# Kernel optimization log

Measured on AMD Instinct MI355X. Metric: run time of the kernel, lower is better.

Reference implementation:

```python
import jax, jax.numpy as jnp
import numpy as np

BIG = 1000000.0


def setup_inputs() -> dict:
    key = jax.random.key(0)
    k1, k2 = jax.random.split(key)
    embeddings = jax.random.normal(k1, (8192, 128), dtype=jnp.float32)
    labels = jax.random.randint(k2, (8192,), 0, 512, dtype=jnp.int64)
    return {"embeddings": embeddings, "labels": labels, "margin": jnp.float32(0.5)}


def _pairwise_euclidean(x):
    # [N, N] Euclidean distance matrix, numerically safe sqrt (zero diag)
    sq = jnp.sum(x * x, axis=1)
    d2 = sq[:, None] + sq[None, :] - 2.0 * (x @ x.T)
    d2 = jnp.maximum(d2, 0.0)
    nz = d2 > 0.0
    return jnp.where(nz, jnp.sqrt(jnp.where(nz, d2, 1.0)), 0.0)


def reference(embeddings, labels, margin):
    n = embeddings.shape[0]
    dist = _pairwise_euclidean(embeddings)                      # [N, N]
    same = (labels[:, None] == labels[None, :]).astype(dist.dtype)
    mask_pos = same - jnp.eye(n, dtype=dist.dtype)              # positives, excl. self
    mask_neg = 1.0 - same                                       # different label
    pos_dist = jnp.max(dist * mask_pos, axis=1)                 # hardest positive
    neg_dist = jnp.min(dist + (1.0 - mask_neg) * BIG, axis=1)   # hardest negative
    loss = jax.nn.relu(pos_dist - neg_dist + margin)
    return jnp.mean(loss)
```

## Files before the change

kernel.cpp:

```cpp
#include <hip/hip_runtime.h>

#define NROW 8192
#define DIM  128
#define NSEG 16
#define NBLK (64 * NSEG)
#define BIGF 1e30f

typedef __attribute__((ext_vector_type(8))) short bf16x8;
typedef __attribute__((ext_vector_type(4))) float f32x4;


__device__ __forceinline__ unsigned short f2bf(float f) {
    unsigned u = __float_as_uint(f);
    unsigned r = (u + 0x7fffu + ((u >> 16) & 1u)) >> 16;
    return (unsigned short)r;
}

__device__ __forceinline__ void gload_lds16(const void* g, void* l) {
    __builtin_amdgcn_global_load_lds(
        (const __attribute__((address_space(1))) void*)g,
        (__attribute__((address_space(3))) void*)l, 16, 0, 0);
}

__global__ __launch_bounds__(256) void prep_kernel(const float* __restrict__ x,
                                                   unsigned short* __restrict__ xb2,
                                                   float* __restrict__ sq,
                                                   float* __restrict__ out) {
    const int t   = threadIdx.x;
    const int row = blockIdx.x * 16 + (t >> 4);
    const int c   = t & 15;
    if (blockIdx.x == 0 && t == 0) out[0] = 0.0f;
    const float* xr = x + (size_t)row * DIM + c * 8;
    float4 f0 = *(const float4*)xr;
    float4 f1 = *(const float4*)(xr + 4);
    float s = f0.x*f0.x + f0.y*f0.y + f0.z*f0.z + f0.w*f0.w
            + f1.x*f1.x + f1.y*f1.y + f1.z*f1.z + f1.w*f1.w;
    #pragma unroll
    for (int m = 1; m <= 8; m <<= 1) s += __shfl_xor(s, m);
    unsigned w0 = (unsigned)f2bf(f0.x) | ((unsigned)f2bf(f0.y) << 16);
    unsigned w1 = (unsigned)f2bf(f0.z) | ((unsigned)f2bf(f0.w) << 16);
    unsigned w2 = (unsigned)f2bf(f1.x) | ((unsigned)f2bf(f1.y) << 16);
    unsigned w3 = (unsigned)f2bf(f1.z) | ((unsigned)f2bf(f1.w) << 16);
    uint4 v = make_uint4(w0, w1, w2, w3);
    *(uint4*)(xb2 + (size_t)(row >> 4) * 2048 + c * 128 + (row & 15) * 8) = v;
    if (c == 0) sq[row] = s;
}

__global__ __launch_bounds__(256, 3) void tile_mfma(const unsigned short* __restrict__ xb2,
                                                    const int* __restrict__ lbl,
                                                    const float* __restrict__ sq,
                                                    float* __restrict__ posS,
                                                    float* __restrict__ negS) {
    __shared__ unsigned short Bs[2][64 * DIM];
    const int bid = blockIdx.x;
    const int rb  = bid >> 4;
    const int jq  = bid & 15;
    const int i0  = rb * 128;
    const int jbase = jq * 512;
    const int t    = threadIdx.x;
    const int lane = t & 63;
    const int w    = t >> 6;
    const int wr0  = i0 + w * 32;
    const int quad = lane >> 4;
    const int l15  = lane & 15;

    const char* xbB = (const char*)xb2;

    bf16x8 af[2][4];
    const int gA = wr0 >> 4;
    #pragma unroll
    for (int ti = 0; ti < 2; ti++)
        #pragma unroll
        for (int ks = 0; ks < 4; ks++)
            af[ti][ks] = *(const bf16x8*)(xb2 + (size_t)(gA + ti) * 2048 + (ks * 4 + quad) * 128 + l15 * 8);

    int lbli[2][4];
    #pragma unroll
    for (int ti = 0; ti < 2; ti++) {
        int4 l4 = *(const int4*)(lbl + wr0 + ti * 16 + quad * 4);
        lbli[ti][0] = l4.x; lbli[ti][1] = l4.y; lbli[ti][2] = l4.z; lbli[ti][3] = l4.w;
    }
    const bool hasDiag = (i0 >= jbase) && (i0 < jbase + 512);

    float posm[2][4], negm[2][4];
    #pragma unroll
    for (int ti = 0; ti < 2; ti++)
        #pragma unroll
        for (int r = 0; r < 4; r++) { posm[ti][r] = -BIGF; negm[ti][r] = BIGF; }

    {
        const char* src = xbB + (size_t)(jbase >> 4) * 4096;
        #pragma unroll
        for (int i = 0; i < 4; i++)
            gload_lds16(src + i * 4096 + t * 16, (char*)&Bs[0][0] + i * 4096 + w * 1024);
    }
    __syncthreads();

    #pragma unroll 1
    for (int jt = 0; jt < 8; jt++) {
        const int cur = jt & 1;
        const int j0  = jbase + jt * 64;

        if (jt < 7) {
            const char* src = xbB + (size_t)((j0 + 64) >> 4) * 4096;
            #pragma unroll
            for (int i = 0; i < 4; i++)
                gload_lds16(src + i * 4096 + t * 16, (char*)&Bs[cur ^ 1][0] + i * 4096 + w * 1024);
        }

        float sqj[4]; int lblj[4];
        #pragma unroll
        for (int tj = 0; tj < 4; tj++) {
            int c = j0 + tj * 16 + l15;
            sqj[tj]  = sq[c];
            lblj[tj] = lbl[c];
        }

        f32x4 acc[2][4];
        #pragma unroll
        for (int ti = 0; ti < 2; ti++)
            #pragma unroll
            for (int tj = 0; tj < 4; tj++) acc[ti][tj] = (f32x4){0.f, 0.f, 0.f, 0.f};

        #pragma unroll
        for (int ks = 0; ks < 4; ks++) {
            bf16x8 bfr[4];
            #pragma unroll
            for (int tj = 0; tj < 4; tj++)
                bfr[tj] = *(const bf16x8*)((const char*)&Bs[cur][0] + tj * 4096 + (ks * 4 + quad) * 256 + l15 * 16);
            #pragma unroll
            for (int ti = 0; ti < 2; ti++)
                #pragma unroll
                for (int tj = 0; tj < 4; tj++)
                    acc[ti][tj] = __builtin_amdgcn_mfma_f32_16x16x32_bf16(af[ti][ks], bfr[tj], acc[ti][tj], 0, 0, 0);
        }

        #pragma unroll
        for (int ti = 0; ti < 2; ti++) {
            const int rowg = wr0 + ti * 16 + quad * 4;
            #pragma unroll
            for (int tj = 0; tj < 4; tj++) {
                const int jc = j0 + tj * 16 + l15;
                #pragma unroll
                for (int r = 0; r < 4; r++) {
                    float sr = fmaf(-2.0f, acc[ti][tj][r], sqj[tj]);
                    bool same = (lbli[ti][r] == lblj[tj]);
                    bool self = hasDiag && (jc == rowg + r);
                    posm[ti][r] = fmaxf(posm[ti][r], (same && !self) ? sr : -BIGF);
                    negm[ti][r] = fminf(negm[ti][r], same ? BIGF : sr);
                }
            }
        }

        __syncthreads();
    }

    #pragma unroll
    for (int ti = 0; ti < 2; ti++)
        #pragma unroll
        for (int r = 0; r < 4; r++) {
            float p = posm[ti][r];
            float n = negm[ti][r];
            #pragma unroll
            for (int m = 8; m >= 1; m >>= 1) {
                p = fmaxf(p, __shfl_xor(p, m));
                n = fminf(n, __shfl_xor(n, m));
            }
            if (l15 == 0) {
                int row = wr0 + ti * 16 + quad * 4 + r;
                float sqi = sq[row];
                posS[jq * NROW + row] = fmaxf(0.0f, sqi + p);
                negS[jq * NROW + row] = fmaxf(0.0f, sqi + n);
            }
        }
}

__global__ __launch_bounds__(256) void tri_final(const float* __restrict__ posS,
                                                 const float* __restrict__ negS,
                                                 const float* __restrict__ margin,
                                                 float* __restrict__ out) {
    int r = blockIdx.x * 256 + threadIdx.x;
    float p = 0.0f, n = BIGF;
    #pragma unroll
    for (int q = 0; q < NSEG; q++) {
        p = fmaxf(p, posS[q * NROW + r]);
        n = fminf(n, negS[q * NROW + r]);
    }
    float m = margin[0];
    float loss = fmaxf(sqrtf(p) - sqrtf(n) + m, 0.0f) * (1.0f / (float)NROW);
    #pragma unroll
    for (int o = 32; o > 0; o >>= 1) loss += __shfl_down(loss, o);
    __shared__ float wsum[4];
    int lane = threadIdx.x & 63, wv = threadIdx.x >> 6;
    if (lane == 0) wsum[wv] = loss;
    __syncthreads();
    if (threadIdx.x == 0) atomicAdd(out, wsum[0] + wsum[1] + wsum[2] + wsum[3]);
}

extern "C" void kernel_launch(void* const* d_in, const int* in_sizes, int n_in,
                              void* d_out, int out_size, void* d_ws, size_t ws_size,
                              hipStream_t stream) {
    const float* x      = (const float*)d_in[0];
    const int*   lbl    = (const int*)d_in[1];
    const float* margin = (const float*)d_in[2];
    float* out = (float*)d_out;

    char* ws = (char*)d_ws;
    unsigned short* xb2 = (unsigned short*)ws;
    float* sq   = (float*)(ws + (2u << 20));
    float* posS = (float*)(ws + (2u << 20) + (64u << 10));
    float* negS = (float*)(ws + (2u << 20) + (576u << 10));

    prep_kernel<<<NROW / 16, 256, 0, stream>>>(x, xb2, sq, out);
    tile_mfma<<<NBLK, 256, 0, stream>>>(xb2, lbl, sq, posS, negS);
    tri_final<<<NROW / 256, 256, 0, stream>>>(posS, negS, margin, out);
}
```

Baseline: 88.77 us.

## Triple-buffer B tiles with explicit vmcnt waits and specialize non-diagonal epilogue

The B-tile staging in LDS grows from double to triple buffering. Loads are issued two tiles ahead, and each iteration waits with a partial s_waitcnt vmcnt plus a raw s_barrier instead of a full __syncthreads, so global-to-LDS copies overlap more with the MFMA work. The distance epilogue is also split on hasDiag, so blocks that contain no diagonal skip the per-element self-comparison. The cost is 48KB of LDS per block, which may limit occupancy, and hand-written waitcnt counts that must match the issued loads.

```diff
diff --git a/kernel.cpp b/kernel.cpp
--- a/kernel.cpp
+++ b/kernel.cpp
@@ -51,7 +51,7 @@
                                                     const float* __restrict__ sq,
                                                     float* __restrict__ posS,
                                                     float* __restrict__ negS) {
-    __shared__ unsigned short Bs[2][64 * DIM];
+    __shared__ unsigned short Bs[3][64 * DIM];
     const int bid = blockIdx.x;
     const int rb  = bid >> 4;
     const int jq  = bid & 15;
@@ -88,24 +88,31 @@
         #pragma unroll
         for (int r = 0; r < 4; r++) { posm[ti][r] = -BIGF; negm[ti][r] = BIGF; }
 
-    {
-        const char* src = xbB + (size_t)(jbase >> 4) * 4096;
-        #pragma unroll
-        for (int i = 0; i < 4; i++)
-            gload_lds16(src + i * 4096 + t * 16, (char*)&Bs[0][0] + i * 4096 + w * 1024);
-    }
-    __syncthreads();
+    #pragma unroll
+    for (int i = 0; i < 4; i++)
+        gload_lds16(xbB + (size_t)(jbase >> 4) * 4096 + i * 4096 + t * 16,
+                    (char*)&Bs[0][0] + i * 4096 + w * 1024);
+    #pragma unroll
+    for (int i = 0; i < 4; i++)
+        gload_lds16(xbB + (size_t)((jbase + 64) >> 4) * 4096 + i * 4096 + t * 16,
+                    (char*)&Bs[1][0] + i * 4096 + w * 1024);
+    __builtin_amdgcn_sched_barrier(0);
+    asm volatile("s_waitcnt vmcnt(4)" ::: "memory");
+    __builtin_amdgcn_sched_barrier(0);
+    __builtin_amdgcn_s_barrier();
+    __builtin_amdgcn_sched_barrier(0);
 
     #pragma unroll 1
     for (int jt = 0; jt < 8; jt++) {
-        const int cur = jt & 1;
+        const int cur = jt % 3;
         const int j0  = jbase + jt * 64;
 
-        if (jt < 7) {
-            const char* src = xbB + (size_t)((j0 + 64) >> 4) * 4096;
+        if (jt < 6) {
+            const char* src = xbB + (size_t)((j0 + 128) >> 4) * 4096;
+            char* dst = (char*)&Bs[(jt + 2) % 3][0];
             #pragma unroll
             for (int i = 0; i < 4; i++)
-                gload_lds16(src + i * 4096 + t * 16, (char*)&Bs[cur ^ 1][0] + i * 4096 + w * 1024);
+                gload_lds16(src + i * 4096 + t * 16, dst + i * 4096 + w * 1024);
         }
 
         float sqj[4]; int lblj[4];
@@ -135,24 +142,45 @@
                     acc[ti][tj] = __builtin_amdgcn_mfma_f32_16x16x32_bf16(af[ti][ks], bfr[tj], acc[ti][tj], 0, 0, 0);
         }
 
-        #pragma unroll
-        for (int ti = 0; ti < 2; ti++) {
-            const int rowg = wr0 + ti * 16 + quad * 4;
-            #pragma unroll
-            for (int tj = 0; tj < 4; tj++) {
-                const int jc = j0 + tj * 16 + l15;
+        if (hasDiag) {
+            #pragma unroll
+            for (int ti = 0; ti < 2; ti++) {
+                const int rowg = wr0 + ti * 16 + quad * 4;
                 #pragma unroll
-                for (int r = 0; r < 4; r++) {
-                    float sr = fmaf(-2.0f, acc[ti][tj][r], sqj[tj]);
-                    bool same = (lbli[ti][r] == lblj[tj]);
-                    bool self = hasDiag && (jc == rowg + r);
-                    posm[ti][r] = fmaxf(posm[ti][r], (same && !self) ? sr : -BIGF);
-                    negm[ti][r] = fminf(negm[ti][r], same ? BIGF : sr);
+                for (int tj = 0; tj < 4; tj++) {
+                    const int jc = j0 + tj * 16 + l15;
+                    #pragma unroll
+                    for (int r = 0; r < 4; r++) {
+                        float sr = fmaf(-2.0f, acc[ti][tj][r], sqj[tj]);
+                        bool same = (lbli[ti][r] == lblj[tj]);
+                        bool self = (jc == rowg + r);
+                        posm[ti][r] = fmaxf(posm[ti][r], (same && !self) ? sr : -BIGF);
+                        negm[ti][r] = fminf(negm[ti][r], same ? BIGF : sr);
+                    }
                 }
             }
-        }
-
-        __syncthreads();
+        } else {
+            #pragma unroll
+            for (int ti = 0; ti < 2; ti++)
+                #pragma unroll
+                for (int tj = 0; tj < 4; tj++)
+                    #pragma unroll
+                    for (int r = 0; r < 4; r++) {
+                        float sr = fmaf(-2.0f, acc[ti][tj][r], sqj[tj]);
+                        bool same = (lbli[ti][r] == lblj[tj]);
+                        posm[ti][r] = fmaxf(posm[ti][r], same ? sr : -BIGF);
+                        negm[ti][r] = fminf(negm[ti][r], same ? BIGF : sr);
+                    }
+        }
+
+        if (jt < 7) {
+            __builtin_amdgcn_sched_barrier(0);
+            if (jt < 6) asm volatile("s_waitcnt vmcnt(4)" ::: "memory");
+            else        asm volatile("s_waitcnt vmcnt(0)" ::: "memory");
+            __builtin_amdgcn_sched_barrier(0);
+            __builtin_amdgcn_s_barrier();
+            __builtin_amdgcn_sched_barrier(0);
+        }
     }
 
     #pragma unroll
```

Result: slower. 92.86 us (+4.6%).

## Load B fragments directly from global memory, drop LDS staging and barriers

Applied to the files above, without the earlier changes.

Removes the double-buffered LDS staging of the column tile and the per-iteration __syncthreads, so each wave reads its B fragments straight from global memory (served by L2/L1). It raises the occupancy hint to 4 blocks per CU and splits the epilogue into a diagonal and a non-diagonal path so most tiles skip the self-comparison. The cost is four times more global/cache traffic, since all four waves of a block fetch the same B tile, and no explicit prefetch to hide load latency behind the MFMAs.

```diff
diff --git a/kernel.cpp b/kernel.cpp
--- a/kernel.cpp
+++ b/kernel.cpp
@@ -14,12 +14,6 @@
     unsigned u = __float_as_uint(f);
     unsigned r = (u + 0x7fffu + ((u >> 16) & 1u)) >> 16;
     return (unsigned short)r;
-}
-
-__device__ __forceinline__ void gload_lds16(const void* g, void* l) {
-    __builtin_amdgcn_global_load_lds(
-        (const __attribute__((address_space(1))) void*)g,
-        (__attribute__((address_space(3))) void*)l, 16, 0, 0);
 }
 
 __global__ __launch_bounds__(256) void prep_kernel(const float* __restrict__ x,
@@ -46,12 +40,11 @@
     if (c == 0) sq[row] = s;
 }
 
-__global__ __launch_bounds__(256, 3) void tile_mfma(const unsigned short* __restrict__ xb2,
+__global__ __launch_bounds__(256, 4) void tile_mfma(const unsigned short* __restrict__ xb2,
                                                     const int* __restrict__ lbl,
                                                     const float* __restrict__ sq,
                                                     float* __restrict__ posS,
                                                     float* __restrict__ negS) {
-    __shared__ unsigned short Bs[2][64 * DIM];
     const int bid = blockIdx.x;
     const int rb  = bid >> 4;
     const int jq  = bid & 15;
@@ -64,8 +57,6 @@
     const int quad = lane >> 4;
     const int l15  = lane & 15;
 
-    const char* xbB = (const char*)xb2;
-
     bf16x8 af[2][4];
     const int gA = wr0 >> 4;
     #pragma unroll
@@ -88,25 +79,10 @@
         #pragma unroll
         for (int r = 0; r < 4; r++) { posm[ti][r] = -BIGF; negm[ti][r] = BIGF; }
 
-    {
-        const char* src = xbB + (size_t)(jbase >> 4) * 4096;
-        #pragma unroll
-        for (int i = 0; i < 4; i++)
-            gload_lds16(src + i * 4096 + t * 16, (char*)&Bs[0][0] + i * 4096 + w * 1024);
-    }
-    __syncthreads();
-
     #pragma unroll 1
     for (int jt = 0; jt < 8; jt++) {
-        const int cur = jt & 1;
-        const int j0  = jbase + jt * 64;
-
-        if (jt < 7) {
-            const char* src = xbB + (size_t)((j0 + 64) >> 4) * 4096;
-            #pragma unroll
-            for (int i = 0; i < 4; i++)
-                gload_lds16(src + i * 4096 + t * 16, (char*)&Bs[cur ^ 1][0] + i * 4096 + w * 1024);
-        }
+        const int j0 = jbase + jt * 64;
+        const int gB = j0 >> 4;
 
         float sqj[4]; int lblj[4];
         #pragma unroll
@@ -127,7 +103,7 @@
             bf16x8 bfr[4];
             #pragma unroll
             for (int tj = 0; tj < 4; tj++)
-                bfr[tj] = *(const bf16x8*)((const char*)&Bs[cur][0] + tj * 4096 + (ks * 4 + quad) * 256 + l15 * 16);
+                bfr[tj] = *(const bf16x8*)(xb2 + (size_t)(gB + tj) * 2048 + (ks * 4 + quad) * 128 + l15 * 8);
             #pragma unroll
             for (int ti = 0; ti < 2; ti++)
                 #pragma unroll
@@ -135,24 +111,36 @@
                     acc[ti][tj] = __builtin_amdgcn_mfma_f32_16x16x32_bf16(af[ti][ks], bfr[tj], acc[ti][tj], 0, 0, 0);
         }
 
-        #pragma unroll
-        for (int ti = 0; ti < 2; ti++) {
-            const int rowg = wr0 + ti * 16 + quad * 4;
-            #pragma unroll
-            for (int tj = 0; tj < 4; tj++) {
-                const int jc = j0 + tj * 16 + l15;
+        if (hasDiag) {
+            #pragma unroll
+            for (int ti = 0; ti < 2; ti++) {
+                const int rowg = wr0 + ti * 16 + quad * 4;
                 #pragma unroll
-                for (int r = 0; r < 4; r++) {
-                    float sr = fmaf(-2.0f, acc[ti][tj][r], sqj[tj]);
-                    bool same = (lbli[ti][r] == lblj[tj]);
-                    bool self = hasDiag && (jc == rowg + r);
-                    posm[ti][r] = fmaxf(posm[ti][r], (same && !self) ? sr : -BIGF);
-                    negm[ti][r] = fminf(negm[ti][r], same ? BIGF : sr);
+                for (int tj = 0; tj < 4; tj++) {
+                    const int jc = j0 + tj * 16 + l15;
+                    #pragma unroll
+                    for (int r = 0; r < 4; r++) {
+                        float sr = fmaf(-2.0f, acc[ti][tj][r], sqj[tj]);
+                        bool same = (lbli[ti][r] == lblj[tj]);
+                        bool self = (jc == rowg + r);
+                        posm[ti][r] = fmaxf(posm[ti][r], (same && !self) ? sr : -BIGF);
+                        negm[ti][r] = fminf(negm[ti][r], same ? BIGF : sr);
+                    }
                 }
             }
-        }
-
-        __syncthreads();
+        } else {
+            #pragma unroll
+            for (int ti = 0; ti < 2; ti++)
+                #pragma unroll
+                for (int tj = 0; tj < 4; tj++)
+                    #pragma unroll
+                    for (int r = 0; r < 4; r++) {
+                        float sr = fmaf(-2.0f, acc[ti][tj][r], sqj[tj]);
+                        bool same = (lbli[ti][r] == lblj[tj]);
+                        posm[ti][r] = fmaxf(posm[ti][r], same ? sr : -BIGF);
+                        negm[ti][r] = fminf(negm[ti][r], same ? BIGF : sr);
+                    }
+        }
     }
 
     #pragma unroll
```

Measured after the change: 90.76 us. +2.2%, slower.
